# Performance work log

Hardware: AMD Instinct MI355X
Metric: run time of the kernel (lower is better)

## Reference

```python
import jax, jax.numpy as jnp
import numpy as np

N_ENT = 100000
N_USR = 30000
N_TOT = N_ENT + N_USR
N_REL = 32
D = 64
E = 500000
INTER = 500000
N_LAYERS = 2
SLOPE = 0.01  # torch nn.LeakyReLU default negative slope


def _seg_softmax(logits, seg, n):
    # sparse softmax over rows (segments)
    m = jax.ops.segment_max(logits, seg, num_segments=n)
    ex = jnp.exp(logits - m[seg])
    den = jax.ops.segment_sum(ex, seg, num_segments=n)
    return ex / den[seg]


def setup_inputs() -> dict:
    key = jax.random.key(0)
    k = jax.random.split(key, 14)
    all_embed = jax.random.normal(k[0], (N_TOT, D), jnp.float32) * 0.1
    rel_embed = jax.random.normal(k[1], (N_REL, D), jnp.float32) * 0.1
    Wk_w = jax.random.normal(k[2], (D, 2 * D), jnp.float32) / np.sqrt(2 * D)
    Wk_b = jnp.zeros((D,), jnp.float32)
    Wa_w = jax.random.normal(k[3], (D, D), jnp.float32) / np.sqrt(D)
    Wb_w = jax.random.normal(k[4], (D, D), jnp.float32) / np.sqrt(D)
    # KG edge lists (head entity, tail entity, relation)
    h_list = jnp.sort(jax.random.randint(k[5], (E,), 0, N_ENT))
    t_list = jax.random.randint(k[6], (E,), 0, N_ENT)
    r_list = jax.random.randint(k[7], (E,), 0, N_REL)
    # bipartite interaction matrix A_in (symmetric, items rows first then users)
    u = jax.random.randint(k[8], (INTER,), 0, N_USR)
    it = jax.random.randint(k[9], (INTER,), 0, N_ENT)
    a_row = jnp.concatenate([it, N_ENT + u])
    a_col = jnp.concatenate([N_ENT + u, it])
    a_vals = jax.random.uniform(k[10], (2 * INTER,), jnp.float32) * 0.01
    # calc_score ids: user ids are offset by n_entities in the concatenated table
    user_ids = N_ENT + jax.random.randint(k[11], (1024,), 0, N_USR)
    item_ids = jax.random.randint(k[12], (2048,), 0, N_ENT)
    return dict(all_embed=all_embed, rel_embed=rel_embed, Wk_w=Wk_w, Wk_b=Wk_b,
                Wa_w=Wa_w, Wb_w=Wb_w, a_vals=a_vals, user_ids=user_ids,
                item_ids=item_ids, h_list=h_list, t_list=t_list, r_list=r_list,
                a_row=a_row, a_col=a_col)


def _get_embeddings(all_embed, rel_embed, Wk_w, Wk_b, Wa_w, Wb_w, a_vals,
                    h_list, t_list, r_list, a_row, a_col):
    e_ent = all_embed[:N_ENT]
    e_usr = all_embed[N_ENT:]
    user_list = [e_usr]
    item_list = [e_ent]
    e_items_dual = e_ent
    e_users_curr = e_usr
    e_ent_curr = e_ent
    r_e = rel_embed[r_list]  # (E, D) -- constant across layers
    for _ in range(N_LAYERS):
        # --- KG attention (Eq. 2): gather + concat + linear + dot + leakyrelu ---
        h_e = e_ent_curr[h_list]            # (E, D)
        t_e = e_ent_curr[t_list]            # (E, D)
        cat = jnp.concatenate([t_e, h_e], axis=1)   # (E, 2D)
        trans = cat @ Wk_w.T + Wk_b                 # (E, D)
        logits = jnp.sum(trans * r_e, axis=1)       # (E,)
        vals = jnp.where(logits >= 0, logits, SLOPE * logits)
        alpha = _seg_softmax(vals, h_list, N_ENT)   # row-wise sparse softmax
        # --- KG aggregation (Eq. 1): spmm ---
        e_items_kg = jax.ops.segment_sum(alpha[:, None] * t_e, h_list,
                                         num_segments=N_ENT)
        # --- IG aggregation (Eq. 3 & 6): spmm with A_in ---
        ig_in = jnp.concatenate([e_items_dual, e_users_curr], axis=0)  # (N_TOT, D)
        ig_out = jax.ops.segment_sum(a_vals[:, None] * ig_in[a_col], a_row,
                                     num_segments=N_TOT)
        e_items_collab = ig_out[:N_ENT]
        e_users_new = ig_out[N_ENT:]
        # --- fusion gate (Eq. 4, 5) ---
        g = jax.nn.sigmoid(e_items_kg @ Wa_w.T + e_items_collab @ Wb_w.T)
        e_items_dual = g * e_items_kg + (1.0 - g) * e_items_collab
        item_list.append(e_items_collab)
        user_list.append(e_users_new)
        e_users_curr = e_users_new
        e_ent_curr = e_items_kg
    item_final = sum(item_list)
    user_final = sum(user_list)
    return jnp.concatenate([item_final, user_final], axis=0)


def reference(all_embed, rel_embed, Wk_w, Wk_b, Wa_w, Wb_w, a_vals,
              user_ids, item_ids, h_list, t_list, r_list, a_row, a_col):
    all_final = _get_embeddings(all_embed, rel_embed, Wk_w, Wk_b, Wa_w, Wb_w,
                                a_vals, h_list, t_list, r_list, a_row, a_col)
    user_e = all_final[user_ids]   # (Bu, D)
    item_e = all_final[item_ids]   # (Bi, D)
    return user_e @ item_e.T       # (Bu, Bi)
```

## Files before the change

kernel.cpp:

```cpp
#include <hip/hip_runtime.h>
#include <hip/hip_bf16.h>

#define N_ENT 100000
#define N_USR 30000
#define N_TOTN 130000
#define N_RELC 32
#define DIM 64
#define NEDGE 500000
#define INTER 500000
#define NA 1000000
#define SLOPE 0.01f
#define SCAN_NB 508
#define CPT_NB 127
#define ATT_NB 1024

typedef unsigned char u8;
typedef unsigned long long u64;

__device__ __forceinline__ float grp_sum16(float v){
  v += __shfl_xor(v, 8, 64);
  v += __shfl_xor(v, 4, 64);
  v += __shfl_xor(v, 2, 64);
  v += __shfl_xor(v, 1, 64);
  return v;
}
__device__ __forceinline__ float grp_max16(float v){
  v = fmaxf(v, __shfl_xor(v, 8, 64));
  v = fmaxf(v, __shfl_xor(v, 4, 64));
  v = fmaxf(v, __shfl_xor(v, 2, 64));
  v = fmaxf(v, __shfl_xor(v, 1, 64));
  return v;
}

__global__ void __launch_bounds__(256) k_prep(
    const float* __restrict__ rel, const float* __restrict__ Wk,
    const float* __restrict__ Wkb, float* __restrict__ m, float* __restrict__ b,
    const int* __restrict__ h_list, int* __restrict__ off,
    const int* __restrict__ user_ids, const int* __restrict__ item_ids,
    u8* __restrict__ r2_item, u8* __restrict__ r2_user){
  int bid = blockIdx.x;
  if (bid < 17){
    int idx = bid*256 + threadIdx.x;
    if (idx < N_RELC*128){
      int r = idx >> 7, j = idx & 127;
      float s = 0.f;
      for (int d = 0; d < DIM; ++d) s += rel[r*DIM+d] * Wk[d*128+j];
      m[idx] = s;
    } else if (idx < N_RELC*128 + N_RELC){
      int r = idx - N_RELC*128;
      float s = 0.f;
      for (int d = 0; d < DIM; ++d) s += Wkb[d] * rel[r*DIM+d];
      b[r] = s;
    }
  } else if (bid < 29){
    int i = (bid - 17)*256 + threadIdx.x;
    if (i < 1024) r2_user[user_ids[i] - N_ENT] = 1;
    else if (i < 3072) r2_item[item_ids[i - 1024]] = 1;
  } else {
    int e = (bid - 29)*256 + threadIdx.x;
    if (e <= NEDGE){
      int hc = (e < NEDGE) ? h_list[e] : N_ENT;
      int hp = (e == 0) ? -1 : h_list[e-1];
      for (int s = hp+1; s <= hc; ++s) off[s] = e;
    }
  }
}

__global__ void k_mark(const int* __restrict__ a_row, const int* __restrict__ a_col,
                       const u8* __restrict__ r2_item, const u8* __restrict__ r2_user,
                       u8* __restrict__ need_d, u8* __restrict__ need_u){
  int i = blockIdx.x*256 + threadIdx.x;
  if (i >= INTER) return;
  int it = a_row[i];
  int uu = a_col[i] - N_ENT;
  if (r2_item[it]) need_u[uu] = 1;
  if (r2_user[uu]) need_d[it] = 1;
}

__global__ void __launch_bounds__(256) k_build(
    const int* __restrict__ a_row, const int* __restrict__ a_col,
    const u8* __restrict__ need_d, const u8* __restrict__ need_u,
    const u8* __restrict__ r2_item, const u8* __restrict__ r2_user,
    int* __restrict__ list_gate, int* __restrict__ list_s1,
    int* __restrict__ counters, int* __restrict__ cnt){
  if (blockIdx.x < CPT_NB){
    __shared__ u64 mg_sh[16], ms_sh[16];
    __shared__ int pre_g[16], pre_s[16];
    __shared__ int base_sh[2];
    int t = threadIdx.x;
    int wave = t >> 6, lane = t & 63;
    bool pg[4], ps[4];
    int ibase = blockIdx.x*1024;
    #pragma unroll
    for (int k = 0; k < 4; ++k){
      int i = ibase + k*256 + t;
      bool g = false, s = false;
      if (i < N_TOTN){
        if (i < N_ENT){ g = need_d[i] != 0; s = g || (r2_item[i] != 0); }
        else { int u = i - N_ENT; s = (need_u[u] != 0) || (r2_user[u] != 0); }
      }
      pg[k] = g; ps[k] = s;
      u64 mg = __ballot(g), ms = __ballot(s);
      if (lane == 0){ mg_sh[k*4 + wave] = mg; ms_sh[k*4 + wave] = ms; }
    }
    __syncthreads();
    if (t == 0){
      int sg = 0, ss = 0;
      for (int j = 0; j < 16; ++j){
        pre_g[j] = sg; sg += __popcll(mg_sh[j]);
        pre_s[j] = ss; ss += __popcll(ms_sh[j]);
      }
      base_sh[0] = sg ? atomicAdd(&counters[0], sg) : 0;
      base_sh[1] = ss ? atomicAdd(&counters[1], ss) : 0;
    }
    __syncthreads();
    int bg = base_sh[0], bs = base_sh[1];
    u64 lmask = (1ull << lane) - 1;
    #pragma unroll
    for (int k = 0; k < 4; ++k){
      int i = ibase + k*256 + t;
      if (pg[k]) list_gate[bg + pre_g[k*4+wave] + __popcll(mg_sh[k*4+wave] & lmask)] = i;
      if (ps[k]) list_s1 [bs + pre_s[k*4+wave] + __popcll(ms_sh[k*4+wave] & lmask)] = i;
    }
  } else {
    int nb = gridDim.x - CPT_NB;
    for (int i = (blockIdx.x - CPT_NB)*256 + threadIdx.x; i < INTER; i += nb*256){
      int it = a_row[i];
      int uc = a_col[i];
      int uu = uc - N_ENT;
      if (need_d[it] | r2_item[it]) atomicAdd(&cnt[it], 1);
      if (need_u[uu] | r2_user[uu]) atomicAdd(&cnt[uc], 1);
    }
  }
}

__global__ void k_scan1(const int* __restrict__ cnt, int* __restrict__ part){
  __shared__ int sh[256];
  int idx = blockIdx.x*256 + threadIdx.x;
  sh[threadIdx.x] = (idx < N_TOTN) ? cnt[idx] : 0;
  __syncthreads();
  for (int o = 128; o > 0; o >>= 1){
    if (threadIdx.x < o) sh[threadIdx.x] += sh[threadIdx.x + o];
    __syncthreads();
  }
  if (threadIdx.x == 0) part[blockIdx.x] = sh[0];
}

__global__ void k_scan3(int* __restrict__ cnt, const int* __restrict__ part,
                        int* __restrict__ row_ptr){
  __shared__ int sh[256];
  int t = threadIdx.x;
  int s = 0;
  for (int j = t; j < blockIdx.x; j += 256) s += part[j];
  sh[t] = s;
  __syncthreads();
  for (int o = 128; o > 0; o >>= 1){
    if (t < o) sh[t] += sh[t + o];
    __syncthreads();
  }
  int base = sh[0];
  __syncthreads();
  int idx = blockIdx.x*256 + t;
  int v = (idx < N_TOTN) ? cnt[idx] : 0;
  sh[t] = v;
  __syncthreads();
  for (int o = 1; o < 256; o <<= 1){
    int a = (t >= o) ? sh[t - o] : 0;
    __syncthreads();
    sh[t] += a;
    __syncthreads();
  }
  int excl = base + sh[t] - v;
  if (idx < N_TOTN){ row_ptr[idx] = excl; cnt[idx] = excl; }
}

__global__ void k_fill(const int* __restrict__ a_row, const int* __restrict__ a_col,
                       const float* __restrict__ a_vals,
                       const u8* __restrict__ need_d, const u8* __restrict__ need_u,
                       const u8* __restrict__ r2_item, const u8* __restrict__ r2_user,
                       int* __restrict__ pos, int* __restrict__ csr_col, float* __restrict__ csr_val){
  int i = blockIdx.x*256 + threadIdx.x;
  if (i >= INTER) return;
  int it = a_row[i];
  int uc = a_col[i];
  int uu = uc - N_ENT;
  if (need_d[it] | r2_item[it]){
    int p = atomicAdd(&pos[it], 1);
    csr_col[p] = uc;
    csr_val[p] = a_vals[i];
  }
  if (need_u[uu] | r2_user[uu]){
    int p = atomicAdd(&pos[uc], 1);
    csr_col[p] = it;
    csr_val[p] = a_vals[i + INTER];
  }
}

__global__ void __launch_bounds__(256) k_l1(const float4* __restrict__ ent4,
    const float4* __restrict__ m4, const float* __restrict__ bvec,
    const int* __restrict__ off, const int* __restrict__ t_list,
    const int* __restrict__ r_list, const int* __restrict__ list_gate,
    const int* __restrict__ list_s1, const int* __restrict__ counters,
    float4* __restrict__ kg4,
    const int* __restrict__ row_ptr, const int* __restrict__ cnt_end,
    const int* __restrict__ csr_col, const float* __restrict__ csr_val,
    float4* __restrict__ collab4, float4* __restrict__ x2_4){
  if (blockIdx.x < ATT_NB){
    __shared__ float4 msh[N_RELC*32];
    __shared__ float bsh[N_RELC];
    for (int i = threadIdx.x; i < N_RELC*32; i += 256) msh[i] = m4[i];
    if (threadIdx.x < N_RELC) bsh[threadIdx.x] = bvec[threadIdx.x];
    __syncthreads();
    int n = counters[0];
    int sub = threadIdx.x & 15;
    int grp = (blockIdx.x*256 + threadIdx.x) >> 4;
    int ng = (ATT_NB*256) >> 4;
    for (int idx = grp; idx < n; idx += ng){
      int s = list_gate[idx];
      int beg = off[s], end = off[s+1];
      float4 h4 = ent4[(size_t)s*16 + sub];
      float run_m = -INFINITY, run_l = 0.f;
      float4 acc = {0.f,0.f,0.f,0.f};
      for (int base = beg; base < end; base += 16){
        int mch = end - base; if (mch > 16) mch = 16;
        int tj = 0, rj = 0;
        if (sub < mch){ tj = t_list[base + sub]; rj = r_list[base + sub]; }
        float logit_mine = -INFINITY;
        #pragma unroll 4
        for (int j = 0; j < mch; ++j){
          int ti = __shfl(tj, j, 16);
          int r  = __shfl(rj, j, 16);
          float4 t4 = ent4[(size_t)ti*16 + sub];
          float4 mt = msh[r*32 + sub];
          float4 mh = msh[r*32 + 16 + sub];
          float v = t4.x*mt.x + t4.y*mt.y + t4.z*mt.z + t4.w*mt.w
                  + h4.x*mh.x + h4.y*mh.y + h4.z*mh.z + h4.w*mh.w;
          v = grp_sum16(v) + bsh[r];
          v = (v >= 0.f) ? v : SLOPE * v;
          if (sub == j) logit_mine = v;
        }
        float cmax = grp_max16(logit_mine);
        float nm = fmaxf(run_m, cmax);
        float al = __expf(run_m - nm);
        run_l *= al;
        acc.x *= al; acc.y *= al; acc.z *= al; acc.w *= al;
        #pragma unroll 4
        for (int j = 0; j < mch; ++j){
          float lg = __shfl(logit_mine, j, 16);
          int ti = __shfl(tj, j, 16);
          float w = __expf(lg - nm);
          float4 t4 = ent4[(size_t)ti*16 + sub];
          run_l += w;
          acc.x += w*t4.x; acc.y += w*t4.y; acc.z += w*t4.z; acc.w += w*t4.w;
        }
        run_m = nm;
      }
      float inv = (end > beg) ? 1.f / run_l : 0.f;
      float4 o = {acc.x*inv, acc.y*inv, acc.z*inv, acc.w*inv};
      kg4[(size_t)s*16 + sub] = o;
    }
  } else {
    int n = counters[1];
    int sub = threadIdx.x & 15;
    int bid = blockIdx.x - ATT_NB;
    int nb = gridDim.x - ATT_NB;
    int grp = (bid*256 + threadIdx.x) >> 4;
    int ng = (nb*256) >> 4;
    for (int idx = grp; idx < n; idx += ng){
      int i = list_s1[idx];
      int beg = row_ptr[i], end = cnt_end[i];
      float4 acc = {0.f,0.f,0.f,0.f};
      for (int base = beg; base < end; base += 16){
        int mch = end - base; if (mch > 16) mch = 16;
        int c = 0; float v = 0.f;
        if (sub < mch){ c = csr_col[base + sub]; v = csr_val[base + sub]; }
        #pragma unroll 4
        for (int j = 0; j < mch; ++j){
          int cj = __shfl(c, j, 16);
          float vj = __shfl(v, j, 16);
          float4 sv = ent4[(size_t)cj*16 + sub];
          acc.x += vj*sv.x; acc.y += vj*sv.y; acc.z += vj*sv.z; acc.w += vj*sv.w;
        }
      }
      if (i < N_ENT) collab4[(size_t)i*16 + sub] = acc;
      else x2_4[(size_t)i*16 + sub] = acc;
    }
  }
}

__global__ void __launch_bounds__(256) k_gate(const float* __restrict__ kg,
    const float* __restrict__ collab, const float* __restrict__ Wa,
    const float* __restrict__ Wb, float* __restrict__ x2dual,
    const int* __restrict__ list, const int* __restrict__ counters){
  int n = counters[0];
  int row0 = blockIdx.x * 64;
  if (row0 >= n) return;
  __shared__ float Xsh[64][129];
  __shared__ float Wsh[128][65];
  for (int i = threadIdx.x; i < 64*64; i += 256){
    int a = i >> 6, j = i & 63;
    Wsh[j][a] = Wa[i];
    Wsh[64 + j][a] = Wb[i];
  }
  for (int i = threadIdx.x; i < 64*128; i += 256){
    int r = i >> 7, c = i & 127;
    int idx = row0 + r;
    float v = 0.f;
    if (idx < n){
      int row = list[idx];
      v = (c < 64) ? kg[(size_t)row*64 + c] : collab[(size_t)row*64 + (c - 64)];
    }
    Xsh[r][c] = v;
  }
  __syncthreads();
  int ct = threadIdx.x & 15, rt = threadIdx.x >> 4;
  int r0 = rt * 4, c0 = ct * 4;
  float acc[4][4] = {};
  for (int k = 0; k < 128; ++k){
    float w0 = Wsh[k][c0], w1 = Wsh[k][c0+1], w2 = Wsh[k][c0+2], w3 = Wsh[k][c0+3];
    #pragma unroll
    for (int i = 0; i < 4; ++i){
      float x = Xsh[r0+i][k];
      acc[i][0] += x*w0; acc[i][1] += x*w1; acc[i][2] += x*w2; acc[i][3] += x*w3;
    }
  }
  #pragma unroll
  for (int i = 0; i < 4; ++i){
    int idx = row0 + r0 + i;
    if (idx < n){
      int row = list[idx];
      float4 o;
      #pragma unroll
      for (int j = 0; j < 4; ++j){
        int c = c0 + j;
        float g = 1.f / (1.f + __expf(-acc[i][j]));
        float kv = Xsh[r0+i][c];
        float cv = Xsh[r0+i][64 + c];
        (&o.x)[j] = g*kv + (1.f - g)*cv;
      }
      *(float4*)&x2dual[(size_t)row*64 + c0] = o;
    }
  }
}

__global__ void __launch_bounds__(256) k_spmm2g(const int* __restrict__ row_ptr,
    const int* __restrict__ cnt_end, const int* __restrict__ csr_col,
    const float* __restrict__ csr_val, const float* __restrict__ x2,
    const float* __restrict__ all_embed, const float* __restrict__ collab1,
    const int* __restrict__ user_ids, const int* __restrict__ item_ids,
    float* __restrict__ user_e, float* __restrict__ item_e){
  int lane = threadIdx.x & 63;
  int g = (blockIdx.x*256 + threadIdx.x) >> 6;
  if (g >= 3072) return;
  int id;
  float b1;
  if (g < 1024){
    id = user_ids[g];
    b1 = x2[(size_t)id*64 + lane];
  } else {
    id = item_ids[g - 1024];
    b1 = collab1[(size_t)id*64 + lane];
  }
  float acc = all_embed[(size_t)id*64 + lane] + b1;
  int beg = row_ptr[id], end = cnt_end[id];
  for (int base = beg; base < end; base += 64){
    int mch = end - base; if (mch > 64) mch = 64;
    int c = 0; float v = 0.f;
    if (lane < mch){ c = csr_col[base + lane]; v = csr_val[base + lane]; }
    #pragma unroll 4
    for (int j = 0; j < mch; ++j){
      int cj = __shfl(c, j, 64);
      float vj = __shfl(v, j, 64);
      acc += vj * x2[(size_t)cj*64 + lane];
    }
  }
  if (g < 1024) user_e[(size_t)g*64 + lane] = acc;
  else item_e[(size_t)(g - 1024)*64 + lane] = acc;
}

__global__ void __launch_bounds__(256) k_out(const float* __restrict__ ue,
    const float* __restrict__ ie, float* __restrict__ out){
  __shared__ float ash[32][65];
  __shared__ float bsh[32][65];
  int row0 = blockIdx.y * 32, col0 = blockIdx.x * 32;
  for (int i = threadIdx.x; i < 32*64; i += 256){
    int r = i >> 6, c = i & 63;
    ash[r][c] = ue[(size_t)(row0 + r)*DIM + c];
    bsh[r][c] = ie[(size_t)(col0 + r)*DIM + c];
  }
  __syncthreads();
  int tx = threadIdx.x & 15, ty = threadIdx.x >> 4;
  int r0 = ty*2, c0 = tx*2;
  float a00=0.f, a01=0.f, a10=0.f, a11=0.f;
  #pragma unroll
  for (int k = 0; k < 64; ++k){
    float x0 = ash[r0][k], x1 = ash[r0+1][k];
    float y0 = bsh[c0][k], y1 = bsh[c0+1][k];
    a00 += x0*y0; a01 += x0*y1; a10 += x1*y0; a11 += x1*y1;
  }
  float2 o0 = {a00, a01}, o1 = {a10, a11};
  *(float2*)&out[(size_t)(row0 + r0)*2048 + col0 + c0] = o0;
  *(float2*)&out[(size_t)(row0 + r0 + 1)*2048 + col0 + c0] = o1;
}

extern "C" void kernel_launch(void* const* d_in, const int* in_sizes, int n_in,
                              void* d_out, int out_size, void* d_ws, size_t ws_size,
                              hipStream_t stream){
  const float* all_embed = (const float*)d_in[0];
  const float* rel_embed = (const float*)d_in[1];
  const float* Wk_w      = (const float*)d_in[2];
  const float* Wk_b      = (const float*)d_in[3];
  const float* Wa_w      = (const float*)d_in[4];
  const float* Wb_w      = (const float*)d_in[5];
  const float* a_vals    = (const float*)d_in[6];
  const int* user_ids   = (const int*)d_in[7];
  const int* item_ids   = (const int*)d_in[8];
  const int* h_list     = (const int*)d_in[9];
  const int* t_list     = (const int*)d_in[10];
  const int* r_list     = (const int*)d_in[11];
  const int* a_row      = (const int*)d_in[12];
  const int* a_col      = (const int*)d_in[13];
  float* out = (float*)d_out;

  char* p = (char*)d_ws;
  auto alloc = [&](size_t bytes)->void*{
    void* r = (void*)p;
    p += (bytes + 255) & ~(size_t)255;
    return r;
  };
  float* m_rel   = (float*)alloc((size_t)N_RELC*128*4);
  float* b_rel   = (float*)alloc((size_t)N_RELC*4);
  int*   kg_off  = (int*)  alloc((size_t)(N_ENT+1)*4);
  size_t zbytes = (size_t)N_TOTN*4 + 256 + (2*(size_t)N_ENT + 2*(size_t)N_USR);
  char*  zbase  = (char*)alloc(zbytes);
  int*   cnt      = (int*)zbase;
  int*   counters = (int*)(zbase + (size_t)N_TOTN*4);
  u8*    r2_item  = (u8*)(zbase + (size_t)N_TOTN*4 + 256);
  u8*    r2_user  = r2_item + N_ENT;
  u8*    need_d   = r2_user + N_USR;
  u8*    need_u   = need_d + N_ENT;
  int*   row_ptr = (int*)  alloc((size_t)(N_TOTN+1)*4);
  int*   part    = (int*)  alloc((size_t)SCAN_NB*4);
  int*   csr_col = (int*)  alloc((size_t)NA*4);
  float* csr_val = (float*)alloc((size_t)NA*4);
  int*   list_gate = (int*)alloc((size_t)N_ENT*4);
  int*   list_s1   = (int*)alloc((size_t)N_TOTN*4);
  float* kg1     = (float*)alloc((size_t)N_ENT*DIM*4);
  float* collab1 = (float*)alloc((size_t)N_ENT*DIM*4);
  float* x2      = (float*)alloc((size_t)N_TOTN*DIM*4);
  float* user_e  = (float*)alloc((size_t)1024*DIM*4);
  float* item_e  = (float*)alloc((size_t)2048*DIM*4);

  hipMemsetAsync(zbase, 0, zbytes, stream);
  k_prep<<<29 + (NEDGE + 1 + 255)/256, 256, 0, stream>>>(rel_embed, Wk_w, Wk_b,
      m_rel, b_rel, h_list, kg_off, user_ids, item_ids, r2_item, r2_user);
  k_mark<<<(INTER + 255)/256, 256, 0, stream>>>(a_row, a_col, r2_item, r2_user, need_d, need_u);
  k_build<<<CPT_NB + 1024, 256, 0, stream>>>(a_row, a_col, need_d, need_u,
      r2_item, r2_user, list_gate, list_s1, counters, cnt);
  k_scan1<<<SCAN_NB, 256, 0, stream>>>(cnt, part);
  k_scan3<<<SCAN_NB, 256, 0, stream>>>(cnt, part, row_ptr);
  k_fill<<<(INTER + 255)/256, 256, 0, stream>>>(a_row, a_col, a_vals,
      need_d, need_u, r2_item, r2_user, cnt, csr_col, csr_val);

  k_l1<<<ATT_NB + 2048, 256, 0, stream>>>((const float4*)all_embed,
      (const float4*)m_rel, b_rel, kg_off, t_list, r_list, list_gate, list_s1,
      counters, (float4*)kg1, row_ptr, cnt, csr_col, csr_val,
      (float4*)collab1, (float4*)x2);
  k_gate<<<(N_ENT + 63)/64, 256, 0, stream>>>(kg1, collab1, Wa_w, Wb_w, x2,
      list_gate, counters);
  k_spmm2g<<<768, 256, 0, stream>>>(row_ptr, cnt, csr_col, csr_val,
      x2, all_embed, collab1, user_ids, item_ids, user_e, item_e);
  dim3 grid_out(2048/32, 1024/32);
  k_out<<<grid_out, 256, 0, stream>>>(user_e, item_e, out);
}
```

Measured before the change: 224.5 us.

## Replace global scans with sparse row offsets, binary-search KG segments, drop max-shift softmax

New measurement: 231.3 us. +3.0%, slower.

```diff
diff --git a/kernel.cpp b/kernel.cpp
--- a/kernel.cpp
+++ b/kernel.cpp
@@ -10,7 +10,6 @@
 #define INTER 500000
 #define NA 1000000
 #define SLOPE 0.01f
-#define SCAN_NB 508
 #define CPT_NB 127
 #define ATT_NB 1024
 
@@ -24,18 +23,10 @@
   v += __shfl_xor(v, 1, 64);
   return v;
 }
-__device__ __forceinline__ float grp_max16(float v){
-  v = fmaxf(v, __shfl_xor(v, 8, 64));
-  v = fmaxf(v, __shfl_xor(v, 4, 64));
-  v = fmaxf(v, __shfl_xor(v, 2, 64));
-  v = fmaxf(v, __shfl_xor(v, 1, 64));
-  return v;
-}
 
 __global__ void __launch_bounds__(256) k_prep(
     const float* __restrict__ rel, const float* __restrict__ Wk,
     const float* __restrict__ Wkb, float* __restrict__ m, float* __restrict__ b,
-    const int* __restrict__ h_list, int* __restrict__ off,
     const int* __restrict__ user_ids, const int* __restrict__ item_ids,
     u8* __restrict__ r2_item, u8* __restrict__ r2_user){
   int bid = blockIdx.x;
@@ -52,17 +43,10 @@
       for (int d = 0; d < DIM; ++d) s += Wkb[d] * rel[r*DIM+d];
       b[r] = s;
     }
-  } else if (bid < 29){
+  } else {
     int i = (bid - 17)*256 + threadIdx.x;
     if (i < 1024) r2_user[user_ids[i] - N_ENT] = 1;
     else if (i < 3072) r2_item[item_ids[i - 1024]] = 1;
-  } else {
-    int e = (bid - 29)*256 + threadIdx.x;
-    if (e <= NEDGE){
-      int hc = (e < NEDGE) ? h_list[e] : N_ENT;
-      int hp = (e == 0) ? -1 : h_list[e-1];
-      for (int s = hp+1; s <= hc; ++s) off[s] = e;
-    }
   }
 }
 
@@ -134,44 +118,31 @@
   }
 }
 
-__global__ void k_scan1(const int* __restrict__ cnt, int* __restrict__ part){
+__global__ void __launch_bounds__(256) k_off(const int* __restrict__ list_s1,
+    const int* __restrict__ counters, int* __restrict__ cnt,
+    int* __restrict__ row_ptr, int* __restrict__ nnz_ctr){
   __shared__ int sh[256];
-  int idx = blockIdx.x*256 + threadIdx.x;
-  sh[threadIdx.x] = (idx < N_TOTN) ? cnt[idx] : 0;
-  __syncthreads();
-  for (int o = 128; o > 0; o >>= 1){
-    if (threadIdx.x < o) sh[threadIdx.x] += sh[threadIdx.x + o];
-    __syncthreads();
-  }
-  if (threadIdx.x == 0) part[blockIdx.x] = sh[0];
-}
-
-__global__ void k_scan3(int* __restrict__ cnt, const int* __restrict__ part,
-                        int* __restrict__ row_ptr){
-  __shared__ int sh[256];
+  __shared__ int basesh;
   int t = threadIdx.x;
-  int s = 0;
-  for (int j = t; j < blockIdx.x; j += 256) s += part[j];
-  sh[t] = s;
-  __syncthreads();
-  for (int o = 128; o > 0; o >>= 1){
-    if (t < o) sh[t] += sh[t + o];
-    __syncthreads();
-  }
-  int base = sh[0];
-  __syncthreads();
-  int idx = blockIdx.x*256 + t;
-  int v = (idx < N_TOTN) ? cnt[idx] : 0;
-  sh[t] = v;
-  __syncthreads();
-  for (int o = 1; o < 256; o <<= 1){
-    int a = (t >= o) ? sh[t - o] : 0;
-    __syncthreads();
-    sh[t] += a;
-    __syncthreads();
-  }
-  int excl = base + sh[t] - v;
-  if (idx < N_TOTN){ row_ptr[idx] = excl; cnt[idx] = excl; }
+  int n = counters[1];
+  for (int base = blockIdx.x*256; base < n; base += gridDim.x*256){
+    int i = base + t;
+    int row = -1, d = 0;
+    if (i < n){ row = list_s1[i]; d = cnt[row]; }
+    sh[t] = d;
+    __syncthreads();
+    for (int o = 1; o < 256; o <<= 1){
+      int a = (t >= o) ? sh[t-o] : 0;
+      __syncthreads();
+      sh[t] += a;
+      __syncthreads();
+    }
+    if (t == 255) basesh = atomicAdd(nnz_ctr, sh[255]);
+    __syncthreads();
+    int excl = basesh + sh[t] - d;
+    if (i < n){ row_ptr[row] = excl; cnt[row] = excl; }
+    __syncthreads();
+  }
 }
 
 __global__ void k_fill(const int* __restrict__ a_row, const int* __restrict__ a_col,
@@ -198,7 +169,7 @@
 
 __global__ void __launch_bounds__(256) k_l1(const float4* __restrict__ ent4,
     const float4* __restrict__ m4, const float* __restrict__ bvec,
-    const int* __restrict__ off, const int* __restrict__ t_list,
+    const int* __restrict__ h_list, const int* __restrict__ t_list,
     const int* __restrict__ r_list, const int* __restrict__ list_gate,
     const int* __restrict__ list_s1, const int* __restrict__ counters,
     float4* __restrict__ kg4,
@@ -217,45 +188,29 @@
     int ng = (ATT_NB*256) >> 4;
     for (int idx = grp; idx < n; idx += ng){
       int s = list_gate[idx];
-      int beg = off[s], end = off[s+1];
+      int lo = 0, hi = NEDGE;
+      while (lo < hi){ int mid = (lo + hi) >> 1; if (h_list[mid] < s) lo = mid + 1; else hi = mid; }
+      int beg = lo;
+      hi = NEDGE;
+      while (lo < hi){ int mid = (lo + hi) >> 1; if (h_list[mid] <= s) lo = mid + 1; else hi = mid; }
+      int end = lo;
       float4 h4 = ent4[(size_t)s*16 + sub];
-      float run_m = -INFINITY, run_l = 0.f;
+      float l = 0.f;
       float4 acc = {0.f,0.f,0.f,0.f};
-      for (int base = beg; base < end; base += 16){
-        int mch = end - base; if (mch > 16) mch = 16;
-        int tj = 0, rj = 0;
-        if (sub < mch){ tj = t_list[base + sub]; rj = r_list[base + sub]; }
-        float logit_mine = -INFINITY;
-        #pragma unroll 4
-        for (int j = 0; j < mch; ++j){
-          int ti = __shfl(tj, j, 16);
-          int r  = __shfl(rj, j, 16);
-          float4 t4 = ent4[(size_t)ti*16 + sub];
-          float4 mt = msh[r*32 + sub];
-          float4 mh = msh[r*32 + 16 + sub];
-          float v = t4.x*mt.x + t4.y*mt.y + t4.z*mt.z + t4.w*mt.w
-                  + h4.x*mh.x + h4.y*mh.y + h4.z*mh.z + h4.w*mh.w;
-          v = grp_sum16(v) + bsh[r];
-          v = (v >= 0.f) ? v : SLOPE * v;
-          if (sub == j) logit_mine = v;
-        }
-        float cmax = grp_max16(logit_mine);
-        float nm = fmaxf(run_m, cmax);
-        float al = __expf(run_m - nm);
-        run_l *= al;
-        acc.x *= al; acc.y *= al; acc.z *= al; acc.w *= al;
-        #pragma unroll 4
-        for (int j = 0; j < mch; ++j){
-          float lg = __shfl(logit_mine, j, 16);
-          int ti = __shfl(tj, j, 16);
-          float w = __expf(lg - nm);
-          float4 t4 = ent4[(size_t)ti*16 + sub];
-          run_l += w;
-          acc.x += w*t4.x; acc.y += w*t4.y; acc.z += w*t4.z; acc.w += w*t4.w;
-        }
-        run_m = nm;
+      for (int e = beg; e < end; ++e){
+        int ti = t_list[e], r = r_list[e];
+        float4 t4 = ent4[(size_t)ti*16 + sub];
+        float4 mt = msh[r*32 + sub];
+        float4 mh = msh[r*32 + 16 + sub];
+        float v = t4.x*mt.x + t4.y*mt.y + t4.z*mt.z + t4.w*mt.w
+                + h4.x*mh.x + h4.y*mh.y + h4.z*mh.z + h4.w*mh.w;
+        v = grp_sum16(v) + bsh[r];
+        v = (v >= 0.f) ? v : SLOPE * v;
+        float w = __expf(v);
+        l += w;
+        acc.x += w*t4.x; acc.y += w*t4.y; acc.z += w*t4.z; acc.w += w*t4.w;
       }
-      float inv = (end > beg) ? 1.f / run_l : 0.f;
+      float inv = (end > beg) ? 1.f / l : 0.f;
       float4 o = {acc.x*inv, acc.y*inv, acc.z*inv, acc.w*inv};
       kg4[(size_t)s*16 + sub] = o;
     }
@@ -430,7 +385,6 @@
   };
   float* m_rel   = (float*)alloc((size_t)N_RELC*128*4);
   float* b_rel   = (float*)alloc((size_t)N_RELC*4);
-  int*   kg_off  = (int*)  alloc((size_t)(N_ENT+1)*4);
   size_t zbytes = (size_t)N_TOTN*4 + 256 + (2*(size_t)N_ENT + 2*(size_t)N_USR);
   char*  zbase  = (char*)alloc(zbytes);
   int*   cnt      = (int*)zbase;
@@ -439,8 +393,7 @@
   u8*    r2_user  = r2_item + N_ENT;
   u8*    need_d   = r2_user + N_USR;
   u8*    need_u   = need_d + N_ENT;
-  int*   row_ptr = (int*)  alloc((size_t)(N_TOTN+1)*4);
-  int*   part    = (int*)  alloc((size_t)SCAN_NB*4);
+  int*   row_ptr = (int*)  alloc((size_t)N_TOTN*4);
   int*   csr_col = (int*)  alloc((size_t)NA*4);
   float* csr_val = (float*)alloc((size_t)NA*4);
   int*   list_gate = (int*)alloc((size_t)N_ENT*4);
@@ -452,18 +405,17 @@
   float* item_e  = (float*)alloc((size_t)2048*DIM*4);
 
   hipMemsetAsync(zbase, 0, zbytes, stream);
-  k_prep<<<29 + (NEDGE + 1 + 255)/256, 256, 0, stream>>>(rel_embed, Wk_w, Wk_b,
-      m_rel, b_rel, h_list, kg_off, user_ids, item_ids, r2_item, r2_user);
+  k_prep<<<29, 256, 0, stream>>>(rel_embed, Wk_w, Wk_b, m_rel, b_rel,
+      user_ids, item_ids, r2_item, r2_user);
   k_mark<<<(INTER + 255)/256, 256, 0, stream>>>(a_row, a_col, r2_item, r2_user, need_d, need_u);
   k_build<<<CPT_NB + 1024, 256, 0, stream>>>(a_row, a_col, need_d, need_u,
       r2_item, r2_user, list_gate, list_s1, counters, cnt);
-  k_scan1<<<SCAN_NB, 256, 0, stream>>>(cnt, part);
-  k_scan3<<<SCAN_NB, 256, 0, stream>>>(cnt, part, row_ptr);
+  k_off<<<128, 256, 0, stream>>>(list_s1, counters, cnt, row_ptr, &counters[2]);
   k_fill<<<(INTER + 255)/256, 256, 0, stream>>>(a_row, a_col, a_vals,
       need_d, need_u, r2_item, r2_user, cnt, csr_col, csr_val);
 
   k_l1<<<ATT_NB + 2048, 256, 0, stream>>>((const float4*)all_embed,
-      (const float4*)m_rel, b_rel, kg_off, t_list, r_list, list_gate, list_s1,
+      (const float4*)m_rel, b_rel, h_list, t_list, r_list, list_gate, list_s1,
       counters, (float4*)kg1, row_ptr, cnt, csr_col, csr_val,
       (float4*)collab1, (float4*)x2);
   k_gate<<<(N_ENT + 63)/64, 256, 0, stream>>>(kg1, collab1, Wa_w, Wb_w, x2,
```
